# Optimization experiments

Measured on AMD Instinct MI355X. Metric: run time of the kernel, lower is better.

## Reference

```python
import jax, jax.numpy as jnp
import numpy as np
import math

B, S, SD = 8, 256, 768            # batch, seq_len, sent_dim (roberta-base)
L, NH, DH, FF = 12, 12, 64, 3072  # bert layers, heads, head dim, ffn dim
K, D, HC, DPH = 5, 200, 4, 50     # gnn layers, concept_dim, gat heads, dim/head
NNT, NET = 4, 38                  # node / edge types
NN = 200                          # nodes per graph
N = B * NN                        # total nodes
E = 50000                         # edges (before self loops)
IE = 200                          # info-exchange MLP hidden dim
LN_EPS = 1e-12
BN_EPS = 1e-5

def _gelu(x):
    return jax.nn.gelu(x, approximate=False)

def _layer_norm(x, w, b):
    m = jnp.mean(x, -1, keepdims=True)
    v = jnp.mean(jnp.square(x - m), -1, keepdims=True)
    return (x - m) * jax.lax.rsqrt(v + LN_EPS) * w + b

def _bn_eval(x, w, b):
    # untrained BatchNorm1d in eval mode: running_mean=0, running_var=1
    return x * np.float32(1.0 / np.sqrt(1.0 + BN_EPS)) * w + b

def _segment_softmax(scores, seg, num_segments):
    smax = jax.ops.segment_max(scores, seg, num_segments=num_segments)
    ex = jnp.exp(scores - smax[seg])
    den = jax.ops.segment_sum(ex, seg, num_segments=num_segments)
    return ex / (den[seg] + 1e-16)

def setup_inputs():
    key = jax.random.key(0)
    ks = iter(jax.random.split(key, 64))
    def nrm(shape, scale=0.02):
        return jax.random.normal(next(ks), shape, jnp.float32) * scale
    z = lambda s: jnp.zeros(s, jnp.float32)
    o = lambda s: jnp.ones(s, jnp.float32)
    return {
        'hidden_states': nrm((B, S, SD), 1.0),
        'attention_mask': z((B, 1, 1, S)),
        '_X': nrm((N, D), 1.0),
        '_node_feature_extra': nrm((N, D), 1.0),
        'qkv_w': nrm((L, 3, SD, SD)), 'qkv_b': z((L, 3, SD)),
        'attn_out_w': nrm((L, SD, SD)), 'attn_out_b': z((L, SD)),
        'ln1_w': o((L, SD)), 'ln1_b': z((L, SD)),
        'ffn_w1': nrm((L, SD, FF)), 'ffn_b1': z((L, FF)),
        'ffn_w2': nrm((L, FF, SD)), 'ffn_b2': z((L, SD)),
        'ln2_w': o((L, SD)), 'ln2_b': z((L, SD)),
        'ee_w1': nrm((NET + 1 + 2 * NNT, D)), 'ee_b1': z((D,)),
        'ee_bn_w': o((D,)), 'ee_bn_b': z((D,)),
        'ee_w2': nrm((D, D)), 'ee_b2': z((D,)),
        'gat_key_w': nrm((K, 3 * D, D)), 'gat_key_b': z((K, D)),
        'gat_msg_w': nrm((K, 3 * D, D)), 'gat_msg_b': z((K, D)),
        'gat_query_w': nrm((K, 2 * D, D)), 'gat_query_b': z((K, D)),
        'gat_mlp_w1': nrm((K, D, D)), 'gat_mlp_b1': z((K, D)),
        'gat_mlp_bn_w': o((K, D)), 'gat_mlp_bn_b': z((K, D)),
        'gat_mlp_w2': nrm((K, D, D)), 'gat_mlp_b2': z((K, D)),
        'ie_w1': nrm((SD + D, IE)), 'ie_b1': z((IE,)),
        'ie_w2': nrm((IE, SD + D)), 'ie_b2': z((SD + D,)),
        'edge_index': jax.random.randint(next(ks), (2, E), 0, N, dtype=jnp.int32),
        'edge_type': jax.random.randint(next(ks), (E,), 0, NET, dtype=jnp.int32),
        '_node_type': jax.random.randint(next(ks), (N,), 0, NNT, dtype=jnp.int32),
    }

def _forward(hidden_states, attention_mask, _X, _node_feature_extra,
             qkv_w, qkv_b, attn_out_w, attn_out_b, ln1_w, ln1_b,
             ffn_w1, ffn_b1, ffn_w2, ffn_b2, ln2_w, ln2_b,
             ee_w1, ee_b1, ee_bn_w, ee_bn_b, ee_w2, ee_b2,
             gat_key_w, gat_key_b, gat_msg_w, gat_msg_b, gat_query_w, gat_query_b,
             gat_mlp_w1, gat_mlp_b1, gat_mlp_bn_w, gat_mlp_bn_b, gat_mlp_w2, gat_mlp_b2,
             ie_w1, ie_b1, ie_w2, ie_b2,
             edge_index, edge_type, _node_type):
    hs = hidden_states
    dt = hs.dtype
    # ---- edge embeddings (shared edge_encoder => identical every gnn layer) ----
    loop = jnp.arange(N, dtype=edge_index.dtype)
    src = jnp.concatenate([edge_index[0], loop])   # [E+N] with self loops
    tgt = jnp.concatenate([edge_index[1], loop])
    edge_vec = jax.nn.one_hot(edge_type, NET + 1, dtype=dt)
    self_edge_vec = jnp.zeros((N, NET + 1), dt).at[:, NET].set(1.0)
    head_vec = jax.nn.one_hot(_node_type[edge_index[0]], NNT, dtype=dt)
    tail_vec = jax.nn.one_hot(_node_type[edge_index[1]], NNT, dtype=dt)
    self_vec = jax.nn.one_hot(_node_type, NNT, dtype=dt)
    feat = jnp.concatenate([
        jnp.concatenate([edge_vec, head_vec, tail_vec], 1),
        jnp.concatenate([self_edge_vec, self_vec, self_vec], 1)], 0)  # [E+N, 47]
    h = jax.nn.relu(_bn_eval(feat @ ee_w1 + ee_b1, ee_bn_w, ee_bn_b))
    edge_emb = h @ ee_w2 + ee_b2                                       # [E+N, D]
    deg_src = jax.ops.segment_sum(jnp.ones(src.shape, dt), src, num_segments=N)[src]
    scale_q = np.float32(1.0 / math.sqrt(DPH))
    scale_a = np.float32(1.0 / math.sqrt(DH))

    def gat_layer(Xc, g):
        x2 = jnp.concatenate([Xc, _node_feature_extra], 1)             # [N, 2D]
        x_i, x_j = x2[tgt], x2[src]                                    # tgt / src gathers
        key = (jnp.concatenate([x_i, edge_emb], 1) @ gat_key_w[g] + gat_key_b[g]).reshape(-1, HC, DPH)
        msg = (jnp.concatenate([x_j, edge_emb], 1) @ gat_msg_w[g] + gat_msg_b[g]).reshape(-1, HC, DPH)
        qry = (x_j @ gat_query_w[g] + gat_query_b[g]).reshape(-1, HC, DPH) * scale_q
        scores = jnp.sum(qry * key, -1)                                 # [E+N, HC]
        alpha = _segment_softmax(scores, src, N) * deg_src[:, None]     # grouped over src, degree-rescaled
        out = (msg * alpha[..., None]).reshape(-1, HC * DPH)
        aggr = jax.ops.segment_sum(out, tgt, num_segments=N)            # [N, D]
        hm = jax.nn.relu(_bn_eval(aggr @ gat_mlp_w1[g] + gat_mlp_b1[g], gat_mlp_bn_w[g], gat_mlp_bn_b[g]))
        return hm @ gat_mlp_w2[g] + gat_mlp_b2[g]

    Xc = _X
    for i in range(L):
        q = (hs @ qkv_w[i, 0] + qkv_b[i, 0]).reshape(B, S, NH, DH).transpose(0, 2, 1, 3)
        k = (hs @ qkv_w[i, 1] + qkv_b[i, 1]).reshape(B, S, NH, DH).transpose(0, 2, 1, 3)
        v = (hs @ qkv_w[i, 2] + qkv_b[i, 2]).reshape(B, S, NH, DH).transpose(0, 2, 1, 3)
        att = jax.nn.softmax(jnp.einsum('bhqd,bhkd->bhqk', q, k) * scale_a + attention_mask, -1)
        ctx = jnp.einsum('bhqk,bhkd->bhqd', att, v).transpose(0, 2, 1, 3).reshape(B, S, SD)
        attn = _layer_norm(ctx @ attn_out_w[i] + attn_out_b[i] + hs, ln1_w[i], ln1_b[i])
        inter = _gelu(attn @ ffn_w1[i] + ffn_b1[i])
        hs = _layer_norm(inter @ ffn_w2[i] + ffn_b2[i] + attn, ln2_w[i], ln2_b[i])
        if i >= L - K:
            g = i - L + K
            Xc = _gelu(gat_layer(Xc, g))
            Xv = Xc.reshape(B, NN, D)
            cf = jnp.concatenate([hs[:, 0, :], Xv[:, 0, :]], 1)         # [B, SD+D]
            cf = _gelu(cf @ ie_w1 + ie_b1) @ ie_w2 + ie_b2              # ie MLP (residual_ie=0)
            hs = hs.at[:, 0, :].set(cf[:, :SD])
            Xc = Xv.at[:, 0, :].set(cf[:, SD:]).reshape(N, D)
    return hs, Xc

def reference(hidden_states, attention_mask, _X, _node_feature_extra,
              qkv_w, qkv_b, attn_out_w, attn_out_b, ln1_w, ln1_b,
              ffn_w1, ffn_b1, ffn_w2, ffn_b2, ln2_w, ln2_b,
              ee_w1, ee_b1, ee_bn_w, ee_bn_b, ee_w2, ee_b2,
              gat_key_w, gat_key_b, gat_msg_w, gat_msg_b, gat_query_w, gat_query_b,
              gat_mlp_w1, gat_mlp_b1, gat_mlp_bn_w, gat_mlp_bn_b, gat_mlp_w2, gat_mlp_b2,
              ie_w1, ie_b1, ie_w2, ie_b2,
              edge_index, edge_type, _node_type):
    return _forward(hidden_states, attention_mask, _X, _node_feature_extra,
                    qkv_w, qkv_b, attn_out_w, attn_out_b, ln1_w, ln1_b,
                    ffn_w1, ffn_b1, ffn_w2, ffn_b2, ln2_w, ln2_b,
                    ee_w1, ee_b1, ee_bn_w, ee_bn_b, ee_w2, ee_b2,
                    gat_key_w, gat_key_b, gat_msg_w, gat_msg_b, gat_query_w, gat_query_b,
                    gat_mlp_w1, gat_mlp_b1, gat_mlp_bn_w, gat_mlp_bn_b, gat_mlp_w2, gat_mlp_b2,
                    ie_w1, ie_b1, ie_w2, ie_b2,
                    edge_index, edge_type, _node_type)
```

## Files before the change

### kernel.cpp

```cpp
#include <hip/hip_runtime.h>
#include <math.h>

namespace {
constexpr int CB = 8, CS = 256, CSD = 768, CL = 12, CNH = 12, CDH = 64, CFF = 3072;
constexpr int CK = 5, CD = 200, CHC = 4, CDPH = 50, CNNT = 4, CNET = 38;
constexpr int CNN = 200, CN = 1600, CE = 50000, CEN = 51600, CIE = 200;
constexpr int KP200 = 256, KP400 = 448;

constexpr long long OPK   = 0;
constexpr long long OATN  = OPK  + 3145728;
constexpr long long OXC   = OATN + 1572864;
constexpr long long OSC   = OXC  + 320000;
constexpr long long OSMX  = OSC  + 206400;
constexpr long long ODEN  = OSMX + 6400;
constexpr long long OAGG  = ODEN + 6400;
constexpr long long ODEG  = OAGG + 320000;
constexpr long long OQN   = ODEG + 1600;
constexpr long long OKN   = OQN  + 320000;
constexpr long long OMN   = OKN  + 320000;
constexpr long long OCF1  = OMN  + 320000;
constexpr long long OCF2  = OCF1 + 1600;
constexpr long long OEESC = OCF2 + 7744;
constexpr long long OEEBS = OEESC + 200;
constexpr long long OMLSC = OEEBS + 200;
constexpr long long OMLBS = OMLSC + 1000;
constexpr long long ONB   = OMLBS + 1000;
constexpr long long OBF   = ONB + 3000 + 8;

constexpr long long BHSB  = 0;
constexpr long long BATNB = BHSB  + 1572864;
constexpr long long BQKV  = BATNB + 1572864;
constexpr long long BVT   = BQKV  + 4718592;
constexpr long long BCTX  = BVT   + 3145728;
constexpr long long BINT  = BCTX  + 1572864;
constexpr long long BWQKV = BINT  + 6291456;
constexpr long long BWAO  = BWQKV + 1769472;
constexpr long long BWF1  = BWAO  + 589824;
constexpr long long BWF2  = BWF1  + 2359296;
constexpr long long BHEE  = BWF2  + 2359296;
constexpr long long BEEMB = BHEE  + 13238272;
constexpr long long BKEYE = BEEMB + 13238272;
constexpr long long BMSGE = BKEYE + 13238272;
constexpr long long BX2   = BMSGE + 13238272;
constexpr long long BAGG  = BX2   + 745472;
constexpr long long BHM   = BAGG  + 425984;
constexpr long long BGN   = BHM   + 425984;
constexpr long long BGE   = BGN   + 1720320;
constexpr long long BM1   = BGE   + 655360;
constexpr long long BM2   = BM1   + 327680;
constexpr long long BEW2  = BM2   + 327680;
constexpr long long BWALL = BEW2  + 65536;
constexpr long long SQW   = 589824;
constexpr long long SFW   = 2359296;
constexpr long long BAQKV = BWALL;
constexpr long long BAAO  = BAQKV + 36 * SQW;
constexpr long long BAF1  = BAAO  + 12 * SQW;
constexpr long long BAF2  = BAF1  + 12 * SFW;
constexpr long long BEND  = BAF2  + 12 * SFW;
constexpr unsigned long long NEED_BIG = (unsigned long long)OBF * 4ull + (unsigned long long)BEND * 2ull;
}

typedef unsigned short ushort_t;
typedef __attribute__((ext_vector_type(8))) short bh8;
typedef __attribute__((ext_vector_type(4))) float fx4;

__device__ inline unsigned dk_fenc(float f) {
    unsigned u = __float_as_uint(f);
    return (u & 0x80000000u) ? ~u : (u | 0x80000000u);
}
__device__ inline float dk_fdec(unsigned u) {
    return (u & 0x80000000u) ? __uint_as_float(u & 0x7fffffffu) : __uint_as_float(~u);
}
__device__ inline float dk_gelu(float v) {
    return 0.5f * v * (1.0f + erff(v * 0.70710678118654752f));
}
__device__ inline ushort_t dk_f2bf(float f) {
    unsigned u = __float_as_uint(f);
    return (ushort_t)((u + 0x7fffu + ((u >> 16) & 1u)) >> 16);
}
__device__ inline float dk_bf2f(ushort_t h) {
    return __uint_as_float(((unsigned)h) << 16);
}
__device__ __forceinline__ void gl_lds16(const ushort_t* g, ushort_t* l) {
    __builtin_amdgcn_global_load_lds(
        (const __attribute__((address_space(1))) unsigned int*)(g),
        (__attribute__((address_space(3))) unsigned int*)(l), 16, 0, 0);
}

template<int DEPTH, int ACT, bool HAS_SCALE>
__global__ __launch_bounds__(256)
void dk_bgemm(const ushort_t* __restrict__ A, const ushort_t* __restrict__ B,
              const float* __restrict__ bias, long long sBias,
              const float* __restrict__ scale,
              float* __restrict__ Cf, ushort_t* __restrict__ Cb,
              int M, int N, int NPAD, int K,
              int lda, int ldb, int ldcf, int ldcb,
              int innerB, long long sAo, long long sAi, long long sBo, long long sBi,
              long long sCo, long long sCi)
{
    int z = blockIdx.z;
    int zo = z / innerB, zi = z - zo * innerB;
    A += zo * sAo + zi * sAi;
    B += zo * sBo + zi * sBi;
    long long coff = zo * sCo + zi * sCi;
    const float* biasp = bias ? (bias + (long long)z * sBias) : nullptr;

    int gx = gridDim.x, gy = gridDim.y;
    int nwg = gx * gy;
    int wid = blockIdx.y * gx + blockIdx.x;
    int q8 = nwg >> 3, r8 = nwg & 7;
    int xcd = wid & 7, off = wid >> 3;
    int base = (xcd < r8) ? xcd * (q8 + 1) : r8 * (q8 + 1) + (xcd - r8) * q8;
    int lin = base + off;
    int nb, mb;
    if (gy > 4 * gx) { mb = lin / gx; nb = lin - mb * gx; }
    else             { nb = lin / gy; mb = lin - nb * gy; }

    __shared__ __align__(16) ushort_t As[DEPTH * 128 * 64];
    __shared__ __align__(16) ushort_t Bs[DEPTH * 64 * 64];

    int tid = threadIdx.x;
    int l = tid & 63, w = tid >> 6;
    int m0 = mb * 128, n0 = nb * 64;

    int sj = l >> 3, scb = (l & 7) ^ sj;
    const ushort_t* gA[4]; const ushort_t* gB[2];
    int loffA[4], loffB[2];
#pragma unroll
    for (int j = 0; j < 4; j++) {
        int row = w * 32 + j * 8 + sj;
        gA[j] = A + (size_t)(m0 + row) * lda + scb * 8;
        loffA[j] = (w * 4 + j) * 512 + l * 8;
    }
#pragma unroll
    for (int j = 0; j < 2; j++) {
        int row = w * 16 + j * 8 + sj;
        gB[j] = B + (size_t)(n0 + row) * ldb + scb * 8;
        loffB[j] = (w * 2 + j) * 512 + l * 8;
    }

    int lr = l & 15, hi = l >> 4;
    int wm = (w >> 1) * 64, wn = (w & 1) * 32;
    int offA[4][2], offB[2][2];
#pragma unroll
    for (int mi = 0; mi < 4; mi++) {
        int rA = wm + mi * 16 + lr;
#pragma unroll
        for (int ks = 0; ks < 2; ks++) {
            int g = ks * 4 + hi;
            offA[mi][ks] = rA * 128 + ((g ^ (rA & 7)) << 4);
        }
    }
#pragma unroll
    for (int ni = 0; ni < 2; ni++) {
        int rB = wn + ni * 16 + lr;
#pragma unroll
        for (int ks = 0; ks < 2; ks++) {
            int g = ks * 4 + hi;
            offB[ni][ks] = rB * 128 + ((g ^ (rB & 7)) << 4);
        }
    }

    auto stage = [&](int t, int buf) {
        int k0 = t << 6;
        ushort_t* Ab = As + buf * 8192;
        ushort_t* Bb = Bs + buf * 4096;
#pragma unroll
        for (int j = 0; j < 4; j++) gl_lds16(gA[j] + k0, Ab + loffA[j]);
#pragma unroll
        for (int j = 0; j < 2; j++) gl_lds16(gB[j] + k0, Bb + loffB[j]);
    };

    fx4 acc[4][2] = {};
    int NT = K >> 6;
    int npro = NT < DEPTH ? NT : DEPTH;
    for (int d = 0; d < npro; ++d) stage(d, d);

    int cur = 0;
    for (int t = 0; t < NT; ++t) {
        int infl = NT - 1 - t;
        if (infl > DEPTH - 1) infl = DEPTH - 1;
        if (DEPTH >= 3 && infl >= 2) asm volatile("s_waitcnt vmcnt(12)" ::: "memory");
        else if (infl == 1)          asm volatile("s_waitcnt vmcnt(6)" ::: "memory");
        else if (infl == 0)          asm volatile("s_waitcnt vmcnt(0)" ::: "memory");
        __builtin_amdgcn_s_barrier();
        __builtin_amdgcn_sched_barrier(0);

        const char* Ab = (const char*)As + cur * 16384;
        const char* Bb = (const char*)Bs + cur * 8192;
#pragma unroll
        for (int ks = 0; ks < 2; ks++) {
            bh8 af[4], bf[2];
#pragma unroll
            for (int mi = 0; mi < 4; mi++)
                af[mi] = *(const bh8*)(Ab + offA[mi][ks]);
#pragma unroll
            for (int ni = 0; ni < 2; ni++)
                bf[ni] = *(const bh8*)(Bb + offB[ni][ks]);
#pragma unroll
            for (int mi = 0; mi < 4; mi++)
#pragma unroll
                for (int ni = 0; ni < 2; ni++)
                    acc[mi][ni] = __builtin_amdgcn_mfma_f32_16x16x32_bf16(af[mi], bf[ni], acc[mi][ni], 0, 0, 0);
        }
        __builtin_amdgcn_s_barrier();
        if (t + DEPTH < NT) stage(t + DEPTH, cur);
        cur = (cur + 1 == DEPTH) ? 0 : (cur + 1);
    }

    float* cf = Cf ? (Cf + coff) : nullptr;
    ushort_t* cb = Cb ? (Cb + coff) : nullptr;
#pragma unroll
    for (int ni = 0; ni < 2; ni++) {
        int nn = n0 + wn + ni * 16 + lr;
        if (nn >= NPAD) continue;
        bool vn = nn < N;
        float sc = (HAS_SCALE && vn) ? scale[nn] : 1.0f;
        float bi = (biasp && vn) ? biasp[nn] : 0.0f;
#pragma unroll
        for (int mi = 0; mi < 4; mi++) {
#pragma unroll
            for (int r = 0; r < 4; r++) {
                int mm = m0 + wm + mi * 16 + hi * 4 + r;
                if (mm >= M) continue;
                float v = 0.0f;
                if (vn) {
                    v = acc[mi][ni][r];
                    if (HAS_SCALE) v *= sc;
                    v += bi;
                    if (ACT == 1) v = fmaxf(v, 0.f);
                    if (ACT == 2) v = dk_gelu(v);
                }
                if (cf && vn) cf[(size_t)mm * ldcf + nn] = v;
                if (cb) cb[(size_t)mm * ldcb + nn] = dk_f2bf(v);
            }
        }
    }
}

__global__ __launch_bounds__(256)
void dk_fattn(const ushort_t* __restrict__ qg, const ushort_t* __restrict__ kg,
              const ushort_t* __restrict__ vg, const float* __restrict__ mask,
              ushort_t* __restrict__ ctx)
{
    int sb = blockIdx.x, z = blockIdx.y;
    int b = z / CNH, h = z - b * CNH;

    __shared__ __align__(16) ushort_t Ks[256 * 64];
    __shared__ __align__(16) ushort_t Vs[64 * 256];

    int tid = threadIdx.x, l = tid & 63, w = tid >> 6;
    int lr = l & 15, hi = l >> 4;

    bh8 vreg[8];
    {
        const ushort_t* vrow = vg + ((size_t)b * 256 + tid) * CSD + h * 64;
#pragma unroll
        for (int j = 0; j < 8; j++) vreg[j] = *(const bh8*)(vrow + j * 8);
    }
    {
        int sj = l >> 3, c = (l & 7) ^ sj;
        const ushort_t* gkb = kg + ((size_t)b * 256 + w * 64 + sj) * CSD + h * 64 + c * 8;
        ushort_t* lds = Ks + (w * 64) * 64 + l * 8;
#pragma unroll
        for (int j = 0; j < 8; j++)
            gl_lds16(gkb + (size_t)(j * 8) * CSD, lds + j * 8 * 64);
    }
    {
        int c = tid >> 3, r = tid & 7;
#pragma unroll
        for (int j = 0; j < 8; j++)
#pragma unroll
            for (int e = 0; e < 8; e++) {
                int d = j * 8 + e;
                Vs[d * 256 + (((c ^ e) << 3) + r)] = (ushort_t)vreg[j][e];
            }
    }
    bh8 qf0, qf1;
    {
        const ushort_t* qrow = qg + ((size_t)b * 256 + sb * 64 + w * 16 + lr) * CSD + h * 64;
        qf0 = *(const bh8*)(qrow + hi * 8);
        qf1 = *(const bh8*)(qrow + 32 + hi * 8);
    }
    float mv[16];
#pragma unroll
    for (int ni = 0; ni < 16; ni++) mv[ni] = mask[b * 256 + ni * 16 + lr];

    __syncthreads();

    fx4 accs[16] = {};
#pragma unroll
    for (int ks = 0; ks < 2; ks++) {
        bh8 qq = ks ? qf1 : qf0;
#pragma unroll
        for (int ni = 0; ni < 16; ni++) {
            int n = ni * 16 + lr;
            int g = ks * 4 + hi;
            bh8 kf = *(const bh8*)((const char*)Ks + n * 128 + ((g ^ (n & 7)) << 4));
            accs[ni] = __builtin_amdgcn_mfma_f32_16x16x32_bf16(qq, kf, accs[ni], 0, 0, 0);
        }
    }

    float pr[16][4];
#pragma unroll
    for (int r = 0; r < 4; r++) {
        float mx = -1e30f;
#pragma unroll
        for (int ni = 0; ni < 16; ni++) {
            float x = accs[ni][r] * 0.125f + mv[ni];
            pr[ni][r] = x;
            mx = fmaxf(mx, x);
        }
#pragma unroll
        for (int s = 1; s < 16; s <<= 1) mx = fmaxf(mx, __shfl_xor(mx, s, 64));
        float sum = 0.f;
#pragma unroll
        for (int ni = 0; ni < 16; ni++) { float e = expf(pr[ni][r] - mx); pr[ni][r] = e; sum += e; }
#pragma unroll
        for (int s = 1; s < 16; s <<= 1) sum += __shfl_xor(sum, s, 64);
        float inv = 1.0f / sum;
#pragma unroll
        for (int ni = 0; ni < 16; ni++) pr[ni][r] *= inv;
    }

    __syncthreads();

    {
        ushort_t* Pw = Ks + w * 4096;
#pragma unroll
        for (int ni = 0; ni < 16; ni++)
#pragma unroll
            for (int r = 0; r < 4; r++) {
                int q = hi * 4 + r;
                int byt = (q * 512 + (ni * 16 + lr) * 2) ^ ((q & 7) << 4);
                *(ushort_t*)((char*)Pw + byt) = dk_f2bf(pr[ni][r]);
            }
    }

    fx4 acco[4] = {};
    const ushort_t* Pw = Ks + w * 4096;
#pragma unroll
    for (int ks = 0; ks < 8; ks++) {
        int g = ks * 4 + hi;
        bh8 pf = *(const bh8*)((const char*)Pw + lr * 512 + ((g ^ (lr & 7)) << 4));
#pragma unroll
        for (int ni = 0; ni < 4; ni++) {
            int d = ni * 16 + lr;
            bh8 vf = *(const bh8*)((const char*)Vs + d * 512 + ((g ^ (d & 7)) << 4));
            acco[ni] = __builtin_amdgcn_mfma_f32_16x16x32_bf16(pf, vf, acco[ni], 0, 0, 0);
        }
    }

    {
        size_t rowbase = (size_t)b * 256 + sb * 64 + w * 16;
#pragma unroll
        for (int ni = 0; ni < 4; ni++)
#pragma unroll
            for (int r = 0; r < 4; r++) {
                int q = hi * 4 + r;
                ctx[(rowbase + q) * CSD + h * 64 + ni * 16 + lr] = dk_f2bf(acco[ni][r]);
            }
    }
}

__global__ __launch_bounds__(256)
void dk_tcast(const float* __restrict__ in, ushort_t* __restrict__ out,
              int K, int N, int ldin, int Np, int Kp,
              long long sIn, long long sOut)
{
    in  += (long long)blockIdx.z * sIn;
    out += (long long)blockIdx.z * sOut;
    int kb = blockIdx.x * 64, nb = blockIdx.y * 64;
    __shared__ float T[64][65];
    int t = threadIdx.x;
    int x = t & 63;
#pragma unroll
    for (int i = 0; i < 16; ++i) {
        int y = (t >> 6) * 16 + i;
        float v = (kb + y < K && nb + x < N) ? in[(size_t)(kb + y) * ldin + nb + x] : 0.f;
        T[y][x] = v;
    }
    __syncthreads();
#pragma unroll
    for (int i = 0; i < 16; ++i) {
        int y = (t >> 6) * 16 + i;
        int n = nb + y, k = kb + x;
        if (n < Np && k < Kp) out[(size_t)n * Kp + k] = dk_f2bf(T[x][y]);
    }
}

__global__ __launch_bounds__(256)
void dk_ln_row(const float* __restrict__ in, const float* __restrict__ w,
               const float* __restrict__ b, float* __restrict__ out,
               ushort_t* __restrict__ outb)
{
    int row = blockIdx.x, tid = threadIdx.x;
    const float* ip = in + (long long)row * CSD;
    float xv[3];
    float s = 0.f;
#pragma unroll
    for (int t = 0; t < 3; t++) { xv[t] = ip[tid + t * 256]; s += xv[t]; }
    __shared__ float red[256];
    red[tid] = s; __syncthreads();
    for (int st = 128; st; st >>= 1) { if (tid < st) red[tid] += red[tid + st]; __syncthreads(); }
    float mean = red[0] * (1.f / 768.f); __syncthreads();
    float v = 0.f;
#pragma unroll
    for (int t = 0; t < 3; t++) { float d = xv[t] - mean; v += d * d; }
    red[tid] = v; __syncthreads();
    for (int st = 128; st; st >>= 1) { if (tid < st) red[tid] += red[tid + st]; __syncthreads(); }
    float var = red[0] * (1.f / 768.f);
    float rs = 1.0f / sqrtf(var + 1e-12f);
    float* op = out + (long long)row * CSD;
    ushort_t* ob = outb + (long long)row * CSD;
#pragma unroll
    for (int t = 0; t < 3; t++) {
        int c = tid + t * 256;
        float y = (xv[t] - mean) * rs * w[c] + b[c];
        op[c] = y;
        ob[c] = dk_f2bf(y);
    }
}

__global__ __launch_bounds__(256)
void dk_ln_fin(const float* __restrict__ p, const float* __restrict__ bias,
               const float* __restrict__ R, const float* __restrict__ w,
               const float* __restrict__ b, float* __restrict__ out,
               ushort_t* __restrict__ outb)
{
    int row = blockIdx.x, tid = threadIdx.x;
    const float* p0 = p + (long long)row * CSD;
    const float* p1 = p0 + 1572864;
    const float* rp = R + (long long)row * CSD;
    float xv[3];
    float s = 0.f;
#pragma unroll
    for (int t = 0; t < 3; t++) {
        int c = tid + t * 256;
        xv[t] = p0[c] + p1[c] + bias[c] + rp[c];
        s += xv[t];
    }
    __shared__ float red[256];
    red[tid] = s; __syncthreads();
    for (int st = 128; st; st >>= 1) { if (tid < st) red[tid] += red[tid + st]; __syncthreads(); }
    float mean = red[0] * (1.f / 768.f); __syncthreads();
    float v = 0.f;
#pragma unroll
    for (int t = 0; t < 3; t++) { float d = xv[t] - mean; v += d * d; }
    red[tid] = v; __syncthreads();
    for (int st = 128; st; st >>= 1) { if (tid < st) red[tid] += red[tid + st]; __syncthreads(); }
    float var = red[0] * (1.f / 768.f);
    float rs = 1.0f / sqrtf(var + 1e-12f);
    float* op = out + (long long)row * CSD;
    ushort_t* ob = outb + (long long)row * CSD;
#pragma unroll
    for (int t = 0; t < 3; t++) {
        int c = tid + t * 256;
        float y = (xv[t] - mean) * rs * w[c] + b[c];
        op[c] = y;
        ob[c] = dk_f2bf(y);
    }
}

__global__ void dk_copy_f32(const float* __restrict__ a, float* __restrict__ o, long long n)
{
    long long i = (long long)blockIdx.x * 256 + threadIdx.x;
    if (i < n) o[i] = a[i];
}

__global__ void dk_init_hs(const float* __restrict__ in, float* __restrict__ out,
                           ushort_t* __restrict__ outb, long long n)
{
    long long i = (long long)blockIdx.x * 256 + threadIdx.x;
    if (i < n) { float v = in[i]; out[i] = v; outb[i] = dk_f2bf(v); }
}

__global__ void dk_fold_bn(const float* __restrict__ b1, const float* __restrict__ bw,
                           const float* __restrict__ bb, float* __restrict__ sc,
                           float* __restrict__ bs, int n)
{
    int i = blockIdx.x * 256 + threadIdx.x;
    if (i >= n) return;
    float c = 1.0f / sqrtf(1.0f + 1e-5f);
    sc[i] = c * bw[i];
    bs[i] = b1[i] * c * bw[i] + bb[i];
}

__global__ void dk_pack_nbias(const float* __restrict__ q, const float* __restrict__ k,
                              const float* __restrict__ m, float* __restrict__ o)
{
    int i = blockIdx.x * 256 + threadIdx.x;
    if (i >= CK * CD) return;
    int g = i / CD, d = i - g * CD;
    o[g * 600 + d]       = q[i];
    o[g * 600 + 200 + d] = k[i];
    o[g * 600 + 400 + d] = m[i];
}

__global__ __launch_bounds__(256)
void dk_ee_gather(const float* __restrict__ w1, const float* __restrict__ sc,
                  const float* __restrict__ bs, const int* __restrict__ eidx,
                  const int* __restrict__ etyp, const int* __restrict__ ntyp,
                  ushort_t* __restrict__ out)
{
    int e = blockIdx.x, d = threadIdx.x;
    float v = 0.f;
    if (d < CD) {
        int t0, s, t;
        if (e < CE) { t0 = etyp[e]; s = eidx[e]; t = eidx[CE + e]; }
        else        { t0 = CNET; s = t = e - CE; }
        int h0 = ntyp[s], t1 = ntyp[t];
        v = w1[t0 * CD + d] + w1[(CNET + 1 + h0) * CD + d] + w1[(CNET + 1 + CNNT + t1) * CD + d];
        v = fmaxf(v * sc[d] + bs[d], 0.f);
    }
    out[(size_t)e * KP200 + d] = dk_f2bf(v);
}

__global__ void dk_deg_init(float* __restrict__ deg)
{
    int i = blockIdx.x * 256 + threadIdx.x;
    if (i < CN) deg[i] = 1.0f;
}
__global__ void dk_deg_count(const int* __restrict__ eidx, float* __restrict__ deg)
{
    int e = blockIdx.x * 256 + threadIdx.x;
    if (e < CE) atomicAdd(&deg[eidx[e]], 1.0f);
}

__global__ void dk_x2_build(const float* __restrict__ Xc, const float* __restrict__ nfe,
                            ushort_t* __restrict__ x2)
{
    int i = blockIdx.x * 256 + threadIdx.x;
    if (i >= CN * KP400) return;
    int n = i / KP400, d = i - n * KP400;
    float v = (d < CD) ? Xc[(size_t)n * CD + d]
            : (d < 2 * CD ? nfe[(size_t)n * CD + (d - CD)] : 0.f);
    x2[i] = dk_f2bf(v);
}

__global__ void dk_cast_pad(const float* __restrict__ in, ushort_t* __restrict__ out)
{
    int i = blockIdx.x * 256 + threadIdx.x;
    if (i >= CN * KP200) return;
    int r = i / KP200, c = i - r * KP200;
    out[i] = (c < CD) ? dk_f2bf(in[(size_t)r * CD + c]) : 0;
}

__global__ __launch_bounds__(256)
void dk_gat_scores(const float* __restrict__ qryN, const float* __restrict__ keyN,
                   const ushort_t* __restrict__ keyE, const int* __restrict__ eidx,
                   float* __restrict__ scores, unsigned* __restrict__ smax)
{
    long long id = (long long)blockIdx.x * 256 + threadIdx.x;
    if (id >= (long long)CEN * CHC) return;
    int e = (int)(id >> 2), h = (int)(id & 3);
    int s, t;
    if (e < CE) { s = eidx[e]; t = eidx[CE + e]; } else { s = t = e - CE; }
    const float* qp = qryN + (long long)s * CD + h * CDPH;
    const float* kp = keyN + (long long)t * CD + h * CDPH;
    const ushort_t* ke = keyE + (size_t)e * KP200 + h * CDPH;
    float acc = 0.f;
#pragma unroll 10
    for (int d = 0; d < CDPH; d++) acc += qp[d] * (kp[d] + dk_bf2f(ke[d]));
    acc *= 0.14142135623730950488f;
    scores[id] = acc;
    atomicMax(&smax[s * CHC + h], dk_fenc(acc));
}

__global__ __launch_bounds__(256)
void dk_gat_expsum(const unsigned* __restrict__ smax, const int* __restrict__ eidx,
                   float* __restrict__ scores, float* __restrict__ den)
{
    long long id = (long long)blockIdx.x * 256 + threadIdx.x;
    if (id >= (long long)CEN * CHC) return;
    int e = (int)(id >> 2), h = (int)(id & 3);
    int s;
    if (e < CE) s = eidx[e]; else s = e - CE;
    float ex = expf(scores[id] - dk_fdec(smax[s * CHC + h]));
    scores[id] = ex;
    atomicAdd(&den[s * CHC + h], ex);
}

__global__ __launch_bounds__(256)
void dk_gat_aggr(const float* __restrict__ msgN, const ushort_t* __restrict__ msgE,
                 const float* __restrict__ scores, const float* __restrict__ den,
                 const float* __restrict__ deg, const int* __restrict__ eidx,
                 float* __restrict__ aggr)
{
    int e = blockIdx.x, d = threadIdx.x;
    if (d >= CD) return;
    int s, t;
    if (e < CE) { s = eidx[e]; t = eidx[CE + e]; } else { s = t = e - CE; }
    int h = d / CDPH;
    float alpha = scores[(long long)e * CHC + h] / (den[s * CHC + h] + 1e-16f) * deg[s];
    float v = (msgN[(long long)s * CD + d] + dk_bf2f(msgE[(size_t)e * KP200 + d])) * alpha;
    atomicAdd(&aggr[(long long)t * CD + d], v);
}

__global__ __launch_bounds__(256)
void dk_ie_mlp1(const float* __restrict__ hs, const float* __restrict__ Xc,
                const float* __restrict__ w1, const float* __restrict__ b1,
                float* __restrict__ cf1)
{
    int n = threadIdx.x;
    int m = blockIdx.x;
    if (n >= CIE) return;
    const float* h = hs + (long long)m * CS * CSD;
    const float* x = Xc + (long long)m * CNN * CD;
    float a0 = 0.f, a1 = 0.f, a2 = 0.f, a3 = 0.f;
    int k = 0;
    for (; k + 4 <= CSD; k += 4) {
        a0 += h[k]     * w1[(k)     * CIE + n];
        a1 += h[k + 1] * w1[(k + 1) * CIE + n];
        a2 += h[k + 2] * w1[(k + 2) * CIE + n];
        a3 += h[k + 3] * w1[(k + 3) * CIE + n];
    }
    const float* w1x = w1 + (long long)CSD * CIE;
    for (k = 0; k + 4 <= CD; k += 4) {
        a0 += x[k]     * w1x[(k)     * CIE + n];
        a1 += x[k + 1] * w1x[(k + 1) * CIE + n];
        a2 += x[k + 2] * w1x[(k + 2) * CIE + n];
        a3 += x[k + 3] * w1x[(k + 3) * CIE + n];
    }
    float acc = (a0 + a1) + (a2 + a3) + b1[n];
    cf1[(long long)m * CIE + n] = dk_gelu(acc);
}

__global__ __launch_bounds__(256)
void dk_ie_mlp2(const float* __restrict__ cf1, const float* __restrict__ w2,
                const float* __restrict__ b2, float* __restrict__ cf2)
{
    int n = blockIdx.x * 256 + threadIdx.x;
    int m = blockIdx.y;
    const int NO = CSD + CD;
    if (n >= NO) return;
    const float* a = cf1 + (long long)m * CIE;
    float a0 = 0.f, a1 = 0.f, a2 = 0.f, a3 = 0.f;
    for (int k = 0; k + 4 <= CIE; k += 4) {
        a0 += a[k]     * w2[(k)     * NO + n];
        a1 += a[k + 1] * w2[(k + 1) * NO + n];
        a2 += a[k + 2] * w2[(k + 2) * NO + n];
        a3 += a[k + 3] * w2[(k + 3) * NO + n];
    }
    cf2[(long long)m * NO + n] = (a0 + a1) + (a2 + a3) + b2[n];
}

__global__ void dk_cf_scatter(const float* __restrict__ cf2, float* __restrict__ hs,
                              ushort_t* __restrict__ hsb, float* __restrict__ Xc)
{
    int i = blockIdx.x * 256 + threadIdx.x;
    if (i >= CB * (CSD + CD)) return;
    int b = i / (CSD + CD), c = i - b * (CSD + CD);
    float v = cf2[i];
    if (c < CSD) {
        hs[(long long)b * CS * CSD + c] = v;
        hsb[(long long)b * CS * CSD + c] = dk_f2bf(v);
    } else {
        Xc[(long long)b * CNN * CD + (c - CSD)] = v;
    }
}

static void bgemm(hipStream_t st, int mode,
                  const ushort_t* A, const ushort_t* B,
                  const float* bias, long long sBias, const float* scale,
                  float* Cf, ushort_t* Cb,
                  int M, int N, int NPAD, int K, int lda, int ldb, int ldcf, int ldcb,
                  int nz = 1, int innerB = 1,
                  long long sAo = 0, long long sAi = 0, long long sBo = 0, long long sBi = 0,
                  long long sCo = 0, long long sCi = 0)
{
    dim3 grid((NPAD + 63) / 64, (M + 127) / 128, nz), blk(256);
    long long blocks = (long long)grid.x * grid.y * grid.z;
    bool d3 = blocks <= 192;
    if (mode == 0) {
        if (d3) dk_bgemm<3, 0, false><<<grid, blk, 0, st>>>(A, B, bias, sBias, scale, Cf, Cb, M, N, NPAD, K, lda, ldb, ldcf, ldcb, innerB, sAo, sAi, sBo, sBi, sCo, sCi);
        else    dk_bgemm<2, 0, false><<<grid, blk, 0, st>>>(A, B, bias, sBias, scale, Cf, Cb, M, N, NPAD, K, lda, ldb, ldcf, ldcb, innerB, sAo, sAi, sBo, sBi, sCo, sCi);
    } else if (mode == 2) {
        if (d3) dk_bgemm<3, 2, false><<<grid, blk, 0, st>>>(A, B, bias, sBias, scale, Cf, Cb, M, N, NPAD, K, lda, ldb, ldcf, ldcb, innerB, sAo, sAi, sBo, sBi, sCo, sCi);
        else    dk_bgemm<2, 2, false><<<grid, blk, 0, st>>>(A, B, bias, sBias, scale, Cf, Cb, M, N, NPAD, K, lda, ldb, ldcf, ldcb, innerB, sAo, sAi, sBo, sBi, sCo, sCi);
    } else {
        if (d3) dk_bgemm<3, 1, true><<<grid, blk, 0, st>>>(A, B, bias, sBias, scale, Cf, Cb, M, N, NPAD, K, lda, ldb, ldcf, ldcb, innerB, sAo, sAi, sBo, sBi, sCo, sCi);
        else    dk_bgemm<2, 1, true><<<grid, blk, 0, st>>>(A, B, bias, sBias, scale, Cf, Cb, M, N, NPAD, K, lda, ldb, ldcf, ldcb, innerB, sAo, sAi, sBo, sBi, sCo, sCi);
    }
}

static void tcast(hipStream_t st, const float* in, ushort_t* out, int K, int N, int ldin,
                  int Np, int Kp, int nz = 1, long long sIn = 0, long long sOut = 0)
{
    dim3 grid((Kp + 63) / 64, (Np + 63) / 64, nz), blk(256);
    dk_tcast<<<grid, blk, 0, st>>>(in, out, K, N, ldin, Np, Kp, sIn, sOut);
}

extern "C" void kernel_launch(void* const* d_in, const int* in_sizes, int n_in,
                              void* d_out, int out_size, void* d_ws, size_t ws_size,
                              hipStream_t stream)
{
    const float* hidden = (const float*)d_in[0];
    const float* amask  = (const float*)d_in[1];
    const float* Xin    = (const float*)d_in[2];
    const float* nfe    = (const float*)d_in[3];
    const float* qkv_w  = (const float*)d_in[4];
    const float* qkv_b  = (const float*)d_in[5];
    const float* aow    = (const float*)d_in[6];
    const float* aob    = (const float*)d_in[7];
    const float* ln1w   = (const float*)d_in[8];
    const float* ln1b   = (const float*)d_in[9];
    const float* f1w    = (const float*)d_in[10];
    const float* f1b    = (const float*)d_in[11];
    const float* f2w    = (const float*)d_in[12];
    const float* f2b    = (const float*)d_in[13];
    const float* ln2w   = (const float*)d_in[14];
    const float* ln2b   = (const float*)d_in[15];
    const float* eew1   = (const float*)d_in[16];
    const float* eeb1   = (const float*)d_in[17];
    const float* eebnw  = (const float*)d_in[18];
    const float* eebnb  = (const float*)d_in[19];
    const float* eew2   = (const float*)d_in[20];
    const float* eeb2   = (const float*)d_in[21];
    const float* gkw    = (const float*)d_in[22];
    const float* gkb    = (const float*)d_in[23];
    const float* gmw    = (const float*)d_in[24];
    const float* gmb    = (const float*)d_in[25];
    const float* gqw    = (const float*)d_in[26];
    const float* gqb    = (const float*)d_in[27];
    const float* mw1    = (const float*)d_in[28];
    const float* mb1    = (const float*)d_in[29];
    const float* mbnw   = (const float*)d_in[30];
    const float* mbnb   = (const float*)d_in[31];
    const float* mw2    = (const float*)d_in[32];
    const float* mb2    = (const float*)d_in[33];
    const float* iew1   = (const float*)d_in[34];
    const float* ieb1   = (const float*)d_in[35];
    const float* iew2   = (const float*)d_in[36];
    const float* ieb2   = (const float*)d_in[37];
    const int*   eidx   = (const int*)d_in[38];
    const int*   etyp   = (const int*)d_in[39];
    const int*   ntyp   = (const int*)d_in[40];

    float* hs    = (float*)d_out;
    float* XcOut = hs + (long long)CB * CS * CSD;

    float* w = (float*)d_ws;
    float* pk   = w + OPK;
    float* atn  = w + OATN;
    float* Xc   = w + OXC;
    float* scrs = w + OSC;
    unsigned* smax = (unsigned*)(w + OSMX);
    float* den  = w + ODEN;
    float* aggr = w + OAGG;
    float* deg  = w + ODEG;
    float* qryN = w + OQN;
    float* keyN = w + OKN;
    float* msgN = w + OMN;
    float* cf1  = w + OCF1;
    float* cf2  = w + OCF2;
    float* eeSc = w + OEESC;
    float* eeBs = w + OEEBS;
    float* mlSc = w + OMLSC;
    float* mlBs = w + OMLBS;
    float* nbias= w + ONB;

    ushort_t* bb = (ushort_t*)(w + OBF);
    ushort_t* hs_b   = bb + BHSB;
    ushort_t* atn_b  = bb + BATNB;
    ushort_t* qkv_bf = bb + BQKV;
    ushort_t* ctx_b  = bb + BCTX;
    ushort_t* int_b  = bb + BINT;
    ushort_t* wqkvT  = bb + BWQKV;
    ushort_t* waoT   = bb + BWAO;
    ushort_t* wf1T   = bb + BWF1;
    ushort_t* wf2T   = bb + BWF2;
    ushort_t* hee    = bb + BHEE;
    ushort_t* eemb   = bb + BEEMB;
    ushort_t* keyE   = bb + BKEYE;
    ushort_t* msgE   = bb + BMSGE;
    ushort_t* x2_b   = bb + BX2;
    ushort_t* aggr_b = bb + BAGG;
    ushort_t* hm_b   = bb + BHM;
    ushort_t* gnT    = bb + BGN;
    ushort_t* geT    = bb + BGE;
    ushort_t* m1T    = bb + BM1;
    ushort_t* m2T    = bb + BM2;
    ushort_t* eew2T  = bb + BEW2;
    ushort_t* aqkv   = bb + BAQKV;
    ushort_t* aao    = bb + BAAO;
    ushort_t* af1    = bb + BAF1;
    ushort_t* af2    = bb + BAF2;

    const bool bigW = (unsigned long long)ws_size >= NEED_BIG + (16ull << 20);

    const long long HS_N = (long long)CB * CS * CSD;
    const long long XC_N = (long long)CN * CD;

    dk_init_hs<<<(unsigned)((HS_N + 255) / 256), 256, 0, stream>>>(hidden, hs, hs_b, HS_N);
    dk_copy_f32<<<(unsigned)((XC_N + 255) / 256), 256, 0, stream>>>(Xin, Xc, XC_N);
    dk_fold_bn<<<1, 256, 0, stream>>>(eeb1, eebnw, eebnb, eeSc, eeBs, CD);
    dk_fold_bn<<<4, 256, 0, stream>>>(mb1, mbnw, mbnb, mlSc, mlBs, CK * CD);
    dk_pack_nbias<<<4, 256, 0, stream>>>(gqb, gkb, gmb, nbias);

    tcast(stream, eew2, eew2T, CD, CD, CD, KP200, KP200);
    tcast(stream, gqw, gnT + 0,      2 * CD, CD, CD, KP200, KP400, CK, 2LL * CD * CD, 344064LL);
    tcast(stream, gkw, gnT + 114688, 2 * CD, CD, CD, KP200, KP400, CK, 3LL * CD * CD, 344064LL);
    tcast(stream, gmw, gnT + 229376, 2 * CD, CD, CD, KP200, KP400, CK, 3LL * CD * CD, 344064LL);
    tcast(stream, gkw + 2 * CD * CD, geT + 0,     CD, CD, CD, KP200, KP200, CK, 3LL * CD * CD, 131072LL);
    tcast(stream, gmw + 2 * CD * CD, geT + 65536, CD, CD, CD, KP200, KP200, CK, 3LL * CD * CD, 131072LL);
    tcast(stream, mw1, m1T, CD, CD, CD, KP200, KP200, CK, (long long)CD * CD, 65536LL);
    tcast(stream, mw2, m2T, CD, CD, CD, KP200, KP200, CK, (long long)CD * CD, 65536LL);

    if (bigW) {
        tcast(stream, qkv_w, aqkv, CSD, CSD, CSD, CSD, CSD, 36, (long long)CSD * CSD, SQW);
        tcast(stream, aow,  aao,  CSD, CSD, CSD, CSD, CSD, 12, (long long)CSD * CSD, SQW);
        tcast(stream, f1w,  af1,  CSD, CFF, CFF, CFF, CSD, 12, (long long)CSD * CFF, SFW);
        tcast(stream, f2w,  af2,  CFF, CSD, CSD, CSD, CFF, 12, (long long)CFF * CSD, SFW);
    }

    dk_ee_gather<<<CEN, 256, 0, stream>>>(eew1, eeSc, eeBs, eidx, etyp, ntyp, hee);
    bgemm(stream, 0, hee, eew2T, eeb2, 0, nullptr, nullptr, eemb,
          CEN, CD, KP200, KP200, KP200, KP200, 0, KP200);

    dk_deg_init<<<(CN + 255) / 256, 256, 0, stream>>>(deg);
    dk_deg_count<<<(CE + 255) / 256, 256, 0, stream>>>(eidx, deg);

    for (int i = 0; i < CL; i++) {
        const ushort_t *wq, *wa, *w1p, *w2p;
        if (bigW) {
            wq  = aqkv + (long long)i * 3 * SQW;
            wa  = aao  + (long long)i * SQW;
            w1p = af1  + (long long)i * SFW;
            w2p = af2  + (long long)i * SFW;
        } else {
            tcast(stream, qkv_w + (long long)i * 3 * CSD * CSD, wqkvT, CSD, CSD, CSD, CSD, CSD,
                  3, (long long)CSD * CSD, (long long)CSD * CSD);
            tcast(stream, aow + (long long)i * CSD * CSD, waoT, CSD, CSD, CSD, CSD, CSD);
            tcast(stream, f1w + (long long)i * CSD * CFF, wf1T, CSD, CFF, CFF, CFF, CSD);
            tcast(stream, f2w + (long long)i * CFF * CSD, wf2T, CFF, CSD, CSD, CSD, CFF);
            wq = wqkvT; wa = waoT; w1p = wf1T; w2p = wf2T;
        }

        bgemm(stream, 0, hs_b, wq, qkv_b + (long long)i * 3 * CSD, CSD, nullptr,
              nullptr, qkv_bf, 2048, CSD, CSD, CSD, CSD, CSD, 0, CSD,
              3, 1, 0, 0, SQW, 0, (long long)2048 * CSD, 0);
        dk_fattn<<<dim3(4, 96), 256, 0, stream>>>(qkv_bf, qkv_bf + 1572864,
                                                  qkv_bf + 3145728, amask, ctx_b);
        bgemm(stream, 0, ctx_b, wa, nullptr, 0, nullptr, pk, nullptr,
              2048, CSD, CSD, 384, CSD, CSD, CSD, 0,
              2, 1, 384, 0, 384, 0, 1572864, 0);
        dk_ln_fin<<<2048, 256, 0, stream>>>(pk, aob + (long long)i * CSD, hs,
              ln1w + (long long)i * CSD, ln1b + (long long)i * CSD, atn, atn_b);
        bgemm(stream, 2, atn_b, w1p, f1b + (long long)i * CFF, 0, nullptr,
              nullptr, int_b, 2048, CFF, CFF, CSD, CSD, CSD, 0, CFF);
        bgemm(stream, 0, int_b, w2p, nullptr, 0, nullptr, pk, nullptr,
              2048, CSD, CSD, 1536, CFF, CFF, CSD, 0,
              2, 1, 1536, 0, 1536, 0, 1572864, 0);
        dk_ln_fin<<<2048, 256, 0, stream>>>(pk, f2b + (long long)i * CSD, atn,
              ln2w + (long long)i * CSD, ln2b + (long long)i * CSD, hs, hs_b);

        if (i >= CL - CK) {
            int g = i - (CL - CK);
            dk_x2_build<<<(CN * KP400 + 255) / 256, 256, 0, stream>>>(Xc, nfe, x2_b);
            bgemm(stream, 0, x2_b, gnT + (long long)g * 344064,
                  nbias + (long long)g * 600, 200, nullptr,
                  qryN, nullptr, CN, CD, CD, KP400, KP400, KP400, CD, 0,
                  3, 1, 0, 0, 114688, 0, 320000, 0);
            bgemm(stream, 0, eemb, geT + (long long)g * 131072, nullptr, 0, nullptr,
                  nullptr, keyE, CEN, CD, KP200, KP200, KP200, KP200, 0, KP200,
                  2, 1, 0, 0, 65536, 0, 0, 13238272);
            hipMemsetAsync(smax, 0, (size_t)(6400 + 6400 + 320000) * sizeof(float), stream);
            dk_gat_scores<<<(CEN * CHC + 255) / 256, 256, 0, stream>>>(qryN, keyN, keyE, eidx, scrs, smax);
            dk_gat_expsum<<<(CEN * CHC + 255) / 256, 256, 0, stream>>>(smax, eidx, scrs, den);
            dk_gat_aggr<<<CEN, 256, 0, stream>>>(msgN, msgE, scrs, den, deg, eidx, aggr);
            dk_cast_pad<<<(CN * KP200 + 255) / 256, 256, 0, stream>>>(aggr, aggr_b);
            bgemm(stream, 3, aggr_b, m1T + (long long)g * 65536,
                  mlBs + (long long)g * CD, 0, mlSc + (long long)g * CD,
                  nullptr, hm_b, CN, CD, KP200, KP200, KP200, KP200, 0, KP200);
            bgemm(stream, 2, hm_b, m2T + (long long)g * 65536,
                  mb2 + (long long)g * CD, 0, nullptr,
                  Xc, nullptr, CN, CD, CD, KP200, KP200, KP200, CD, 0);
            dk_ie_mlp1<<<CB, 256, 0, stream>>>(hs, Xc, iew1, ieb1, cf1);
            dk_ie_mlp2<<<dim3(4, CB), 256, 0, stream>>>(cf1, iew2, ieb2, cf2);
            dk_cf_scatter<<<(CB * (CSD + CD) + 255) / 256, 256, 0, stream>>>(cf2, hs, hs_b, Xc);
        }
    }

    dk_copy_f32<<<(unsigned)((XC_N + 255) / 256), 256, 0, stream>>>(Xc, XcOut, XC_N);
}
```

Baseline: 2.850 ms.

## Fold edge key projection into per-node query-weight product for GAT scores

Instead of computing an edge key embedding (E x 200) with a GEMM and dotting it with the query, the score kernel now uses q·(W_e·emb) = (W_eᵀ q)·emb. A small per-source-node kernel precomputes q projected through the edge-key weights (4 heads x 200), and the score kernel dots the raw edge embedding with it. This halves the edge GEMM work and drops the keyE buffer writes and reads. The cost is a per-thread 200-long loop per edge with a strided, uncoalesced one-thread-per-edge access pattern, plus changed rounding (fp32 weights, no bf16 keyE).

```diff
diff --git a/kernel.cpp b/kernel.cpp
--- a/kernel.cpp
+++ b/kernel.cpp
@@ -25,7 +25,8 @@
 constexpr long long OMLSC = OEEBS + 200;
 constexpr long long OMLBS = OMLSC + 1000;
 constexpr long long ONB   = OMLBS + 1000;
-constexpr long long OBF   = ONB + 3000 + 8;
+constexpr long long OQW   = ONB + 3000;
+constexpr long long OBF   = OQW + 1280000 + 8;
 
 constexpr long long BHSB  = 0;
 constexpr long long BATNB = BHSB  + 1572864;
@@ -46,7 +47,7 @@
 constexpr long long BHM   = BAGG  + 425984;
 constexpr long long BGN   = BHM   + 425984;
 constexpr long long BGE   = BGN   + 1720320;
-constexpr long long BM1   = BGE   + 655360;
+constexpr long long BM1   = BGE   + 327680;
 constexpr long long BM2   = BM1   + 327680;
 constexpr long long BEW2  = BM2   + 327680;
 constexpr long long BWALL = BEW2  + 65536;
@@ -547,24 +548,67 @@
 }
 
 __global__ __launch_bounds__(256)
+void dk_qw(const float* __restrict__ qryN, const float* __restrict__ gkwE,
+           float* __restrict__ qW)
+{
+    int s = blockIdx.x;
+    int j = threadIdx.x;
+    __shared__ float qls[200];
+    if (j < 200) qls[j] = qryN[(size_t)s * CD + j];
+    __syncthreads();
+    if (j >= 200) return;
+    const float* wr = gkwE + (size_t)j * CD;
+    float a0 = 0.f, a1 = 0.f, a2 = 0.f, a3 = 0.f;
+#pragma unroll 10
+    for (int d = 0; d < 50; d++) {
+        a0 += qls[d]       * wr[d];
+        a1 += qls[50 + d]  * wr[50 + d];
+        a2 += qls[100 + d] * wr[100 + d];
+        a3 += qls[150 + d] * wr[150 + d];
+    }
+    float* o = qW + (size_t)s * 800 + j;
+    o[0]   = a0;
+    o[200] = a1;
+    o[400] = a2;
+    o[600] = a3;
+}
+
+__global__ __launch_bounds__(256)
 void dk_gat_scores(const float* __restrict__ qryN, const float* __restrict__ keyN,
-                   const ushort_t* __restrict__ keyE, const int* __restrict__ eidx,
+                   const float* __restrict__ qW, const ushort_t* __restrict__ eemb,
+                   const int* __restrict__ eidx,
                    float* __restrict__ scores, unsigned* __restrict__ smax)
 {
-    long long id = (long long)blockIdx.x * 256 + threadIdx.x;
-    if (id >= (long long)CEN * CHC) return;
-    int e = (int)(id >> 2), h = (int)(id & 3);
+    int e = blockIdx.x * 256 + threadIdx.x;
+    if (e >= CEN) return;
     int s, t;
     if (e < CE) { s = eidx[e]; t = eidx[CE + e]; } else { s = t = e - CE; }
-    const float* qp = qryN + (long long)s * CD + h * CDPH;
-    const float* kp = keyN + (long long)t * CD + h * CDPH;
-    const ushort_t* ke = keyE + (size_t)e * KP200 + h * CDPH;
-    float acc = 0.f;
+    const float* qp = qryN + (size_t)s * CD;
+    const float* kp = keyN + (size_t)t * CD;
+    const float* qw = qW + (size_t)s * 800;
+    const ushort_t* ep = eemb + (size_t)e * KP200;
+    float acc[4];
+#pragma unroll
+    for (int h = 0; h < 4; h++) {
+        float a = 0.f;
 #pragma unroll 10
-    for (int d = 0; d < CDPH; d++) acc += qp[d] * (kp[d] + dk_bf2f(ke[d]));
-    acc *= 0.14142135623730950488f;
-    scores[id] = acc;
-    atomicMax(&smax[s * CHC + h], dk_fenc(acc));
+        for (int d = 0; d < 50; d++) a += qp[h * 50 + d] * kp[h * 50 + d];
+        acc[h] = a;
+    }
+#pragma unroll 8
+    for (int j = 0; j < 200; j++) {
+        float ej = dk_bf2f(ep[j]);
+        acc[0] += ej * qw[j];
+        acc[1] += ej * qw[200 + j];
+        acc[2] += ej * qw[400 + j];
+        acc[3] += ej * qw[600 + j];
+    }
+#pragma unroll
+    for (int h = 0; h < 4; h++) {
+        float sc = acc[h] * 0.14142135623730950488f;
+        scores[(size_t)e * 4 + h] = sc;
+        atomicMax(&smax[s * CHC + h], dk_fenc(sc));
+    }
 }
 
 __global__ __launch_bounds__(256)
@@ -759,6 +803,7 @@
     float* mlSc = w + OMLSC;
     float* mlBs = w + OMLBS;
     float* nbias= w + ONB;
+    float* qW   = w + OQW;
 
     ushort_t* bb = (ushort_t*)(w + OBF);
     ushort_t* hs_b   = bb + BHSB;
@@ -772,7 +817,6 @@
     ushort_t* wf2T   = bb + BWF2;
     ushort_t* hee    = bb + BHEE;
     ushort_t* eemb   = bb + BEEMB;
-    ushort_t* keyE   = bb + BKEYE;
     ushort_t* msgE   = bb + BMSGE;
     ushort_t* x2_b   = bb + BX2;
     ushort_t* aggr_b = bb + BAGG;
@@ -802,8 +846,7 @@
     tcast(stream, gqw, gnT + 0,      2 * CD, CD, CD, KP200, KP400, CK, 2LL * CD * CD, 344064LL);
     tcast(stream, gkw, gnT + 114688, 2 * CD, CD, CD, KP200, KP400, CK, 3LL * CD * CD, 344064LL);
     tcast(stream, gmw, gnT + 229376, 2 * CD, CD, CD, KP200, KP400, CK, 3LL * CD * CD, 344064LL);
-    tcast(stream, gkw + 2 * CD * CD, geT + 0,     CD, CD, CD, KP200, KP200, CK, 3LL * CD * CD, 131072LL);
-    tcast(stream, gmw + 2 * CD * CD, geT + 65536, CD, CD, CD, KP200, KP200, CK, 3LL * CD * CD, 131072LL);
+    tcast(stream, gmw + 2 * CD * CD, geT, CD, CD, CD, KP200, KP200, CK, 3LL * CD * CD, 65536LL);
     tcast(stream, mw1, m1T, CD, CD, CD, KP200, KP200, CK, (long long)CD * CD, 65536LL);
     tcast(stream, mw2, m2T, CD, CD, CD, KP200, KP200, CK, (long long)CD * CD, 65536LL);
 
@@ -862,11 +905,12 @@
                   nbias + (long long)g * 600, 200, nullptr,
                   qryN, nullptr, CN, CD, CD, KP400, KP400, KP400, CD, 0,
                   3, 1, 0, 0, 114688, 0, 320000, 0);
-            bgemm(stream, 0, eemb, geT + (long long)g * 131072, nullptr, 0, nullptr,
-                  nullptr, keyE, CEN, CD, KP200, KP200, KP200, KP200, 0, KP200,
-                  2, 1, 0, 0, 65536, 0, 0, 13238272);
+            bgemm(stream, 0, eemb, geT + (long long)g * 65536, nullptr, 0, nullptr,
+                  nullptr, msgE, CEN, CD, KP200, KP200, KP200, KP200, 0, KP200);
+            dk_qw<<<CN, 256, 0, stream>>>(qryN,
+                  gkw + (long long)g * 3 * CD * CD + 2LL * CD * CD, qW);
             hipMemsetAsync(smax, 0, (size_t)(6400 + 6400 + 320000) * sizeof(float), stream);
-            dk_gat_scores<<<(CEN * CHC + 255) / 256, 256, 0, stream>>>(qryN, keyN, keyE, eidx, scrs, smax);
+            dk_gat_scores<<<(CEN + 255) / 256, 256, 0, stream>>>(qryN, keyN, qW, eemb, eidx, scrs, smax);
             dk_gat_expsum<<<(CEN * CHC + 255) / 256, 256, 0, stream>>>(smax, eidx, scrs, den);
             dk_gat_aggr<<<CEN, 256, 0, stream>>>(msgN, msgE, scrs, den, deg, eidx, aggr);
             dk_cast_pad<<<(CN * KP200 + 255) / 256, 256, 0, stream>>>(aggr, aggr_b);
```

Result: slower. 3.289 ms (+15.4%).
